# Kernel tuning notes

Measured on AMD Instinct MI355X. Metric: run time of the kernel, lower is better.

Reference implementation:

```python
import jax, jax.numpy as jnp
import numpy as np

V, E, H, D = 50257, 512, 512, 2  # vocab, embed_dim, hidden_dim, depth (nlayers)
B, S, T = 32, 60, 48             # batch, encoder len, target len


def setup_inputs() -> dict:
    key = jax.random.key(0)
    ks = jax.random.split(key, 9)
    return {
        "enc_h": jax.random.normal(ks[0], (B, S, 2 * H), jnp.float32),
        "prev_s": jax.random.normal(ks[1], (B, H), jnp.float32),
        "target": jax.random.randint(ks[2], (T, B), 0, V),
        "embed_W": jax.random.normal(ks[3], (V, E), jnp.float32) * 0.02,
        "attn_W": jax.random.normal(ks[4], (2 * H, H), jnp.float32) * (1.0 / np.sqrt(2 * H)),
        "attn_b": jnp.zeros((H,), jnp.float32),
        "inp_W": jax.random.normal(ks[5], (E, 2 * H), jnp.float32) * (1.0 / np.sqrt(E)),
        "inp_b": jnp.zeros((2 * H,), jnp.float32),
        "cell_W": jax.random.normal(ks[6], (D, H, 2 * H), jnp.float32) * (1.0 / np.sqrt(H)),
        "cell_b": jnp.zeros((D, 2 * H), jnp.float32),
        "out_W": jax.random.normal(ks[7], (H, V), jnp.float32) * (1.0 / np.sqrt(H)),
        "out_b": jnp.zeros((V,), jnp.float32),
    }


def reference(enc_h, prev_s, target, embed_W, attn_W, attn_b,
              inp_W, inp_b, cell_W, cell_b, out_W, out_b):
    # target: T x B -> embeddings T x B x E
    emb = embed_W[target]
    # enc_h is fixed across timesteps: precompute attention keys (B x S x H)
    energy = jnp.tanh(enc_h @ attn_W + attn_b)
    depth = cell_W.shape[0]

    def step(s, x_t):
        # attention: scores B x S, ctx B x 2H
        scores = jnp.einsum("bsh,bh->bs", energy, s)
        alpha = jax.nn.softmax(scores, axis=-1)
        ctx = jnp.einsum("bs,bsd->bd", alpha, enc_h)
        ctx_e = ctx[:, :E]  # module uses ctx[:, 0:embed_dim] (j never updated)
        for l in range(depth):  # small fixed depth loop
            Ws = (s * ctx_e) @ cell_W[l] + cell_b[l]
            if l == 0:
                Ws = Ws + x_t @ inp_W + inp_b
            hh, tt = jnp.split(Ws, 2, axis=1)
            hh = jnp.tanh(hh)
            tt = jax.nn.sigmoid(tt)
            s = hh * tt + s * (1.0 - tt)  # highway gate (dropout p=0)
        return s, s

    _, dec_h = jax.lax.scan(step, prev_s, emb)  # T x B x H
    return dec_h @ out_W + out_b  # T x B x V
```

## Files before the change

### kernel.cpp

```cpp
#include <hip/hip_runtime.h>
#include <hip/hip_bf16.h>
#include <math.h>

#define B_ 32
#define S_ 60
#define T_ 48
#define H_ 512
#define E_ 512
#define V_ 50257
#define NPAD 50432
#define EPI_LD 260

typedef __attribute__((ext_vector_type(8))) short bf16x8v;
typedef __attribute__((ext_vector_type(4))) float f32x4v;
typedef __attribute__((ext_vector_type(4))) float f32x4a __attribute__((aligned(4)));
typedef __attribute__((ext_vector_type(4))) unsigned int u32x4;

__device__ inline unsigned short f2bf(float f) {
    union { float f; unsigned u; } v; v.f = f;
    unsigned r = v.u + 0x7fffu + ((v.u >> 16) & 1u);
    return (unsigned short)(r >> 16);
}
__device__ inline float bflo(unsigned u) { return __uint_as_float(u << 16); }

__device__ inline void gload_lds16(const void* g, void* l) {
    __builtin_amdgcn_global_load_lds(
        (const __attribute__((address_space(1))) unsigned int*)g,
        (__attribute__((address_space(3))) unsigned int*)l, 16, 0, 0);
}

__device__ __forceinline__ u32x4 ld_cohx4(const void* p) {
    u32x4 r;
    asm volatile("global_load_dwordx4 %0, %1, off sc0 sc1"
                 : "=v"(r) : "v"(p) : "memory");
    return r;
}
__device__ __forceinline__ float ld_coh_f32(const float* p) {
    float r;
    asm volatile("global_load_dword %0, %1, off sc0 sc1\n\ts_waitcnt vmcnt(0)"
                 : "=v"(r) : "v"(p) : "memory");
    return r;
}
__device__ __forceinline__ float ld_coh_f32_nw(const float* p) {
    float r;
    asm volatile("global_load_dword %0, %1, off sc0 sc1"
                 : "=v"(r) : "v"(p) : "memory");
    return r;
}
__device__ __forceinline__ void st_coh_f32(float* p, float v) {
    asm volatile("global_store_dword %0, %1, off sc0 sc1"
                 :: "v"(p), "v"(v) : "memory");
}
__device__ __forceinline__ void st_coh_u16(unsigned short* p, unsigned int v) {
    asm volatile("global_store_short %0, %1, off sc0 sc1"
                 :: "v"(p), "v"(v) : "memory");
}
__device__ __forceinline__ void st_coh_u32(int* p, int v) {
    asm volatile("global_store_dword %0, %1, off sc0 sc1"
                 :: "v"(p), "v"(v) : "memory");
}
__device__ __forceinline__ int ld_coh_u32(const int* p) {
    int r;
    asm volatile("global_load_dword %0, %1, off sc0 sc1\n\ts_waitcnt vmcnt(0)"
                 : "=v"(r) : "v"(p) : "memory");
    return r;
}

__device__ __forceinline__ void gbar(int* flags, int idx, int bi) {
    asm volatile("s_waitcnt vmcnt(0)" ::: "memory");
    __syncthreads();
    if (threadIdx.x == 0)
        st_coh_u32(&flags[idx * 32 + bi], 1);
    if (threadIdx.x < 64) {
        const int* fp = &flags[idx * 32 + (threadIdx.x & 31)];
        for (;;) {
            int v = ld_coh_u32(fp);
            if (__all(v != 0)) break;
            __builtin_amdgcn_s_sleep(1);
        }
    }
    __syncthreads();
}

template<int ACT, bool GATHER>
__device__ void gemm_body(const float* __restrict__ A, const float* __restrict__ Bm,
                          const float* __restrict__ bias, float* __restrict__ C,
                          int N, int K, int lda, const int* __restrict__ gidx,
                          int cb, int rb, float (*As)[128], float (*Bs)[128])
{
    const int tid = threadIdx.x;
    const int am = tid >> 1;
    const int ak = (tid & 1) * 4;
    const int arow = rb + am;
    const float* Arow;
    if (GATHER) Arow = A + (size_t)gidx[arow] * lda;
    else        Arow = A + (size_t)arow * lda;

    const int bk = tid >> 5;
    const int bn = (tid & 31) * 4;

    const int tx = tid & 15, ty = tid >> 4;
    float acc[8][8];
    #pragma unroll
    for (int i = 0; i < 8; i++)
        #pragma unroll
        for (int j = 0; j < 8; j++) acc[i][j] = 0.f;

    for (int k0 = 0; k0 < K; k0 += 8) {
        float4 av = *(const float4*)(Arow + k0 + ak);
        float4 bv = *(const float4*)(Bm + (size_t)(k0 + bk) * N + cb + bn);
        __syncthreads();
        As[ak + 0][am] = av.x; As[ak + 1][am] = av.y;
        As[ak + 2][am] = av.z; As[ak + 3][am] = av.w;
        Bs[bk][bn + 0] = bv.x; Bs[bk][bn + 1] = bv.y;
        Bs[bk][bn + 2] = bv.z; Bs[bk][bn + 3] = bv.w;
        __syncthreads();

        #pragma unroll
        for (int k = 0; k < 8; k++) {
            float a[8], b[8];
            *(float4*)(a)     = *(const float4*)&As[k][ty * 4];
            *(float4*)(a + 4) = *(const float4*)&As[k][ty * 4 + 64];
            *(float4*)(b)     = *(const float4*)&Bs[k][tx * 4];
            *(float4*)(b + 4) = *(const float4*)&Bs[k][tx * 4 + 64];
            #pragma unroll
            for (int i = 0; i < 8; i++)
                #pragma unroll
                for (int j = 0; j < 8; j++)
                    acc[i][j] = fmaf(a[i], b[j], acc[i][j]);
        }
    }

    #pragma unroll
    for (int i = 0; i < 8; i++) {
        int row = rb + ((i < 4) ? (ty * 4 + i) : (64 + ty * 4 + (i - 4)));
        #pragma unroll
        for (int j = 0; j < 8; j++) {
            int col = cb + ((j < 4) ? (tx * 4 + j) : (64 + tx * 4 + (j - 4)));
            float v = acc[i][j] + bias[col];
            if (ACT == 1) v = tanhf(v);
            C[(size_t)row * N + col] = v;
        }
    }
}

__global__ __launch_bounds__(256)
void gemm_pro(const float* __restrict__ enc_h, const float* __restrict__ attn_W,
              const float* __restrict__ attn_b, float* __restrict__ energy,
              const float* __restrict__ embed_W, const float* __restrict__ inp_W,
              const float* __restrict__ inp_b, float* __restrict__ pre,
              const int* __restrict__ target, int* __restrict__ cnt)
{
    __shared__ float As[8][128];
    __shared__ float Bs[8][128];
    const int bx = blockIdx.x;
    if (bx < 60) {
        const int cb = (bx & 3) * 128, rb = (bx >> 2) * 128;
        gemm_body<1, false>(enc_h, attn_W, attn_b, energy,
                            512, 1024, 1024, nullptr, cb, rb, As, Bs);
    } else if (bx < 156) {
        const int b2 = bx - 60;
        const int cb = (b2 & 7) * 128, rb = (b2 >> 3) * 128;
        gemm_body<0, true>(embed_W, inp_W, inp_b, pre,
                           1024, 512, 512, target, cb, rb, As, Bs);
    } else {
        for (int i = threadIdx.x; i < 144 * 32; i += 256)
            st_coh_u32(&cnt[i], 0);
    }
}

union __align__(16) ScanSM {
    struct {
        float eL[S_][H_];
        float part[8 * 32 * 36];
        float sCol[512];
    } s;
    float til[2 * 32 * 33];
};

template<int LI>
__device__ __forceinline__ void highway(
    int t, int bi, int tid, int lane, int wv,
    const bf16x8v (&wf)[2][2],
    const unsigned short* __restrict__ xsrc,
    unsigned short* __restrict__ xG1,
    const float* __restrict__ ctxG,
    float* __restrict__ sG,
    unsigned short* __restrict__ dec_b,
    const float* __restrict__ pre,
    float cbh, float cbt,
    float* part, float* sCol)
{
    const int l15 = lane & 15, lc = lane >> 4;
    const int b = tid >> 4, hi = tid & 15;
    const int h = bi * 16 + hi;

    float cxv = 0.f, prh = 0.f, prt = 0.f;
    if (LI == 0) {
        cxv = ld_coh_f32_nw(ctxG + (size_t)b * 512 + h);
        const float* pr = pre + ((size_t)t * B_ + b) * 1024;
        prh = pr[h]; prt = pr[h + 512];
    }

    u32x4 xr[2][2][2];
    #pragma unroll
    for (int ktl = 0; ktl < 2; ++ktl)
        #pragma unroll
        for (int pl = 0; pl < 2; ++pl)
            #pragma unroll
            for (int mt = 0; mt < 2; ++mt) {
                int ch = (((wv * 2 + ktl) * 2 + pl) * 4 + lc) * 32 + mt * 16 + l15;
                xr[ktl][pl][mt] = ld_cohx4(xsrc + (size_t)ch * 8);
            }
    asm volatile("s_waitcnt vmcnt(0)" ::: "memory");
    __builtin_amdgcn_sched_barrier(0);

    f32x4v acc[2][2];
    #pragma unroll
    for (int mt = 0; mt < 2; ++mt)
        #pragma unroll
        for (int nt = 0; nt < 2; ++nt) acc[mt][nt] = (f32x4v)0.f;

    #pragma unroll
    for (int ktl = 0; ktl < 2; ++ktl)
        #pragma unroll
        for (int pl = 0; pl < 2; ++pl)
            #pragma unroll
            for (int mt = 0; mt < 2; ++mt) {
                bf16x8v xv = *(bf16x8v*)&xr[ktl][pl][mt];
                #pragma unroll
                for (int nt = 0; nt < 2; ++nt)
                    acc[mt][nt] = __builtin_amdgcn_mfma_f32_16x16x32_bf16(
                        wf[ktl][nt], xv, acc[mt][nt], 0, 0, 0);
            }

    #pragma unroll
    for (int mt = 0; mt < 2; ++mt)
        #pragma unroll
        for (int nt = 0; nt < 2; ++nt)
            *(f32x4v*)&part[(wv * 32 + mt * 16 + l15) * 36 + nt * 16 + lc * 4] = acc[mt][nt];
    __syncthreads();

    float rh = 0.f, rt = 0.f;
    #pragma unroll
    for (int w = 0; w < 8; ++w) {
        rh += part[(w * 32 + b) * 36 + hi];
        rt += part[(w * 32 + b) * 36 + 16 + hi];
    }
    float ph = rh + cbh, pt = rt + cbt;
    if (LI == 0) { ph += prh; pt += prt; }
    float hh = tanhf(ph);
    float tg = 1.f / (1.f + __expf(-pt));
    float sold = sCol[tid];
    float sn = hh * tg + sold * (1.f - tg);
    sCol[tid] = sn;
    if (LI == 0) {
        float x1 = sn * cxv;
        unsigned short xh = f2bf(x1);
        unsigned short xl = f2bf(x1 - bflo((unsigned)xh));
        int kt = h >> 5, lc2 = (h >> 3) & 3, jj = h & 7;
        int ch = (kt * 8 + lc2) * 32 + b;
        st_coh_u16(xG1 + (size_t)ch * 8 + jj, xh);
        st_coh_u16(xG1 + (size_t)(ch + 128) * 8 + jj, xl);
    } else {
        st_coh_f32(sG + ((size_t)bi * 32 + b) * 16 + hi, sn);
        dec_b[((size_t)bi * 1536 + (size_t)t * B_ + b) * 16 + hi] = f2bf(sn);
    }
}

__global__ __launch_bounds__(512, 2)
void scan_tr(const float* __restrict__ energy, const float* __restrict__ enc_h,
             const float* __restrict__ prev_s, const float* __restrict__ pre,
             const float* __restrict__ cell_W, const float* __restrict__ cell_b,
             unsigned short* __restrict__ dec_b,
             const float* __restrict__ outW, unsigned short* __restrict__ Wt,
             float* __restrict__ ctxG, float* __restrict__ sG,
             unsigned short* __restrict__ xG0, unsigned short* __restrict__ xG1,
             int* __restrict__ cnt)
{
    __shared__ ScanSM sm;
    const int tid = threadIdx.x;

    if (blockIdx.x >= B_) {
        const int hb = blockIdx.x - B_;
        const int g = tid >> 8;
        const int tt0 = tid & 255;
        const int r = tt0 >> 3, c4 = (tt0 & 7) * 4;
        float* til = sm.til;
        #pragma unroll 1
        for (int j = 0; j < 57; ++j) {
            const int tt = hb * 2 + g + j * 448;
            const bool act = tt < (NPAD / 32) * 16;
            int n0 = 0, k0 = 0;
            if (act) {
                n0 = (tt >> 4) * 32;
                k0 = (tt & 15) * 32;
                #pragma unroll
                for (int jj = 0; jj < 4; ++jj) {
                    int n = n0 + c4 + jj;
                    til[(g * 32 + r) * 33 + c4 + jj] =
                        (n < V_) ? __builtin_nontemporal_load(&outW[(size_t)(k0 + r) * V_ + n]) : 0.f;
                }
            }
            __syncthreads();
            if (act) {
                const int n = n0 + r;
                unsigned lo = (unsigned)f2bf(til[(g * 32 + c4 + 0) * 33 + r])
                            | ((unsigned)f2bf(til[(g * 32 + c4 + 1) * 33 + r]) << 16);
                unsigned hi2 = (unsigned)f2bf(til[(g * 32 + c4 + 2) * 33 + r])
                             | ((unsigned)f2bf(til[(g * 32 + c4 + 3) * 33 + r]) << 16);
                unsigned long long ov = (unsigned long long)lo | ((unsigned long long)hi2 << 32);
                __builtin_nontemporal_store(ov, (unsigned long long*)&Wt[(size_t)n * 512 + k0 + c4]);
            }
            __syncthreads();
        }
        return;
    }

    const int bi = blockIdx.x;
    const int lane = tid & 63, wv = tid >> 6;
    float (*eL)[H_] = sm.s.eL;
    float* part   = sm.s.part;
    float* sA     = part;
    float* scoreL = part + 512;
    float* alphaL = part + 576;
    float* sCol   = sm.s.sCol;
    int*   sF     = cnt + 100 * 32;

    for (int i = tid; i < S_ * H_ / 4; i += 512) {
        int s = i >> 7, h4 = (i & 127) * 4;
        *(float4*)&eL[s][h4] = *(const float4*)&energy[((size_t)bi * S_ + s) * 512 + h4];
    }

    bf16x8v wf0[2][2], wf1[2][2];
    {
        const int l15 = lane & 15, lc = lane >> 4;
        #pragma unroll
        for (int ktl = 0; ktl < 2; ++ktl)
            #pragma unroll
            for (int nt = 0; nt < 2; ++nt) {
                const int kb = (wv * 2 + ktl) * 32 + lc * 8;
                const int n  = nt * 512 + bi * 16 + l15;
                #pragma unroll
                for (int jj = 0; jj < 8; ++jj) {
                    wf0[ktl][nt][jj] = (short)f2bf(cell_W[((size_t)(kb + jj)) * 1024 + n]);
                    wf1[ktl][nt][jj] = (short)f2bf(cell_W[((size_t)(512 + kb + jj)) * 1024 + n]);
                }
            }
    }
    const int hME = bi * 16 + (tid & 15);
    sCol[tid] = prev_s[(size_t)(tid >> 4) * 512 + hME];
    const float cb0h = cell_b[hME],        cb0t = cell_b[512 + hME];
    const float cb1h = cell_b[1024 + hME], cb1t = cell_b[1536 + hME];

    #pragma unroll 1
    for (int t = 0; t < T_; ++t) {
        float sAv;
        if (t == 0) {
            sAv = prev_s[(size_t)bi * 512 + tid];
            __syncthreads();
            sA[tid] = sAv;
            __syncthreads();
        } else {
            const int* fp = &sF[tid >> 4];
            for (;;) {
                int v = ld_coh_u32(fp);
                if (v >= t) break;
                __builtin_amdgcn_s_sleep(1);
            }
            sAv = ld_coh_f32_nw(sG + ((size_t)(tid >> 4) * 32 + bi) * 16 + (tid & 15));
            __syncthreads();
            asm volatile("s_waitcnt vmcnt(0)" ::: "memory");
            sA[tid] = sAv;
            __syncthreads();
        }

        #pragma unroll 1
        for (int sp = 0; sp < 4; ++sp) {
            const int s0 = wv + sp * 16;
            const int s1 = s0 + 8;
            const bool has1 = (sp < 3) | (wv < 4);
            const float* e0 = &eL[s0][lane];
            const float* e1 = &eL[has1 ? s1 : s0][lane];
            float a0 = 0.f, a1 = 0.f;
            #pragma unroll
            for (int j = 0; j < 8; ++j) {
                float sv = sA[lane + j * 64];
                a0 = fmaf(e0[j * 64], sv, a0);
                a1 = fmaf(e1[j * 64], sv, a1);
            }
            #pragma unroll
            for (int off = 32; off; off >>= 1) {
                a0 += __shfl_xor(a0, off, 64);
                a1 += __shfl_xor(a1, off, 64);
            }
            if (lane == 0) {
                scoreL[s0] = a0;
                if (has1) scoreL[s1] = a1;
            }
        }
        __syncthreads();
        if (wv == 0) {
            float v = (lane < S_) ? scoreL[lane] : -3.4e38f;
            float m = v;
            #pragma unroll
            for (int off = 32; off; off >>= 1) m = fmaxf(m, __shfl_xor(m, off, 64));
            float e = (lane < S_) ? __expf(v - m) : 0.f;
            float su = e;
            #pragma unroll
            for (int off = 32; off; off >>= 1) su += __shfl_xor(su, off, 64);
            if (lane < S_) alphaL[lane] = e / su;
        }
        __syncthreads();
        {
            float a = 0.f;
            const float* ep = enc_h + (size_t)bi * S_ * 1024 + tid;
            #pragma unroll 20
            for (int s = 0; s < S_; ++s) a = fmaf(alphaL[s], ep[(size_t)s * 1024], a);
            st_coh_f32(ctxG + (size_t)bi * 512 + tid, a);
            float x0 = a * sA[tid];
            unsigned short xh = f2bf(x0);
            unsigned short xl = f2bf(x0 - bflo((unsigned)xh));
            int kt = tid >> 5, lc2 = (tid >> 3) & 3, jj = tid & 7;
            int ch = (kt * 8 + lc2) * 32 + bi;
            st_coh_u16(xG0 + (size_t)ch * 8 + jj, xh);
            st_coh_u16(xG0 + (size_t)(ch + 128) * 8 + jj, xl);
        }
        gbar(cnt, 2 * t + 0, bi);
        highway<0>(t, bi, tid, lane, wv, wf0, xG0, xG1, ctxG, sG, dec_b, pre,
                   cb0h, cb0t, part, sCol);
        gbar(cnt, 2 * t + 1, bi);
        highway<1>(t, bi, tid, lane, wv, wf1, xG1, xG1, ctxG, sG, dec_b, pre,
                   cb1h, cb1t, part, sCol);
        asm volatile("s_waitcnt vmcnt(0)" ::: "memory");
        __syncthreads();
        if (tid == 0)
            st_coh_u32(&sF[bi], t + 1);
    }
}

__global__ __launch_bounds__(512)
void gemm_out(const unsigned short* __restrict__ dec, const unsigned short* __restrict__ Wt,
              const float* __restrict__ bias, float* __restrict__ out)
{
    __shared__ char smem[49152];
    short* As_wt  = (short*)smem;
    short* Bs_dec = (short*)(smem + 32768);
    float* epi    = (float*)smem;

    const int tid = threadIdx.x;
    const int lane = tid & 63, w = tid >> 6;
    const int wm = w >> 2, wn = w & 3;

    const int nwg = (NPAD / 256) * 12;
    const int qx = nwg >> 3, rx = nwg & 7;
    const int xcd = blockIdx.x & 7, idx = blockIdx.x >> 3;
    const int wgid = (xcd < rx ? xcd * (qx + 1) : rx * (qx + 1) + (xcd - rx) * qx) + idx;
    const int rb = (wgid % 12) * 128;
    const int cb = (wgid / 12) * 256;

#define STAGE_TILE(bi, kt) do {                                               \
        short* Ab_ = As_wt + (bi) * 8192;                                     \
        short* Bb_ = Bs_dec + (bi) * 4096;                                    \
        _Pragma("unroll")                                                     \
        for (int j_ = 0; j_ < 2; ++j_) {                                      \
            int rg_ = w * 2 + j_;                                             \
            int row_ = rg_ * 16 + (lane >> 2);                                \
            int kc_ = (lane & 3) ^ (row_ & 3);                                \
            gload_lds16(Wt + ((size_t)(cb + row_) * 512 + (kt) * 32 + kc_ * 8), \
                        Ab_ + rg_ * 512);                                     \
        }                                                                     \
        {                                                                     \
            int row_ = w * 16 + (lane >> 2);                                  \
            int kc_ = (lane & 3) ^ (row_ & 3);                                \
            gload_lds16(dec + (((size_t)((kt) * 2 + (kc_ >> 1)) * 1536 + (rb + row_)) * 16 \
                               + (kc_ & 1) * 8),                              \
                        Bb_ + w * 512);                                       \
        }                                                                     \
    } while (0)

    f32x4v acc[4][4];
    #pragma unroll
    for (int i = 0; i < 4; ++i)
        #pragma unroll
        for (int j = 0; j < 4; ++j) acc[i][j] = (f32x4v)0.f;

    STAGE_TILE(0, 0);

    #pragma unroll 1
    for (int it = 0; it < 16; ++it) {
        const int cur = it & 1;
        __builtin_amdgcn_s_barrier();
        asm volatile("" ::: "memory");
        if (it < 15) {
            STAGE_TILE(cur ^ 1, it + 1);
            asm volatile("s_waitcnt vmcnt(3)" ::: "memory");
        } else {
            asm volatile("s_waitcnt vmcnt(0)" ::: "memory");
        }
        __builtin_amdgcn_s_barrier();
        asm volatile("" ::: "memory");

        const short* Ab = As_wt + cur * 8192;
        const short* Bb = Bs_dec + cur * 4096;
        bf16x8v af[4], bf[4];
        const int lc = lane >> 4;
        #pragma unroll
        for (int ni = 0; ni < 4; ++ni) {
            int r = wn * 64 + ni * 16 + (lane & 15);
            af[ni] = *(const bf16x8v*)&Ab[r * 32 + ((lc ^ (r & 3)) * 8)];
        }
        #pragma unroll
        for (int mi = 0; mi < 4; ++mi) {
            int r = wm * 64 + mi * 16 + (lane & 15);
            bf[mi] = *(const bf16x8v*)&Bb[r * 32 + ((lc ^ (r & 3)) * 8)];
        }
        #pragma unroll
        for (int mi = 0; mi < 4; ++mi)
            #pragma unroll
            for (int ni = 0; ni < 4; ++ni)
                acc[mi][ni] = __builtin_amdgcn_mfma_f32_16x16x32_bf16(
                    af[ni], bf[mi], acc[mi][ni], 0, 0, 0);
    }
#undef STAGE_TILE

    const int c4 = (tid & 63) * 4;
    const bool fullcols = (cb + 256 <= V_);
    f32x4v bq = (f32x4v)0.f;
    if (fullcols) {
        float4 t4 = *(const float4*)(bias + cb + c4);
        bq[0] = t4.x; bq[1] = t4.y; bq[2] = t4.z; bq[3] = t4.w;
    }

    #pragma unroll
    for (int mi = 0; mi < 4; ++mi) {
        __syncthreads();
        #pragma unroll
        for (int ni = 0; ni < 4; ++ni) {
            const int er = wm * 16 + (lane & 15);
            const int ec = wn * 64 + ni * 16 + (lane >> 4) * 4;
            *(f32x4v*)&epi[er * EPI_LD + ec] = acc[mi][ni];
        }
        __syncthreads();
        #pragma unroll
        for (int j = 0; j < 4; ++j) {
            const int rr = w + j * 8;
            const int orow = rb + (rr >> 4) * 64 + mi * 16 + (rr & 15);
            f32x4v v = *(const f32x4v*)&epi[rr * EPI_LD + c4];
            if (fullcols) {
                v += bq;
                *(f32x4a*)(out + (size_t)orow * V_ + cb + c4) = v;
            } else {
                #pragma unroll
                for (int vv = 0; vv < 4; ++vv) {
                    const int col = cb + c4 + vv;
                    if (col < V_)
                        out[(size_t)orow * V_ + col] = v[vv] + bias[col];
                }
            }
        }
    }
}

extern "C" void kernel_launch(void* const* d_in, const int* in_sizes, int n_in,
                              void* d_out, int out_size, void* d_ws, size_t ws_size,
                              hipStream_t stream)
{
    const float* enc_h   = (const float*)d_in[0];
    const float* prev_s  = (const float*)d_in[1];
    const int*   target  = (const int*)  d_in[2];
    const float* embed_W = (const float*)d_in[3];
    const float* attn_W  = (const float*)d_in[4];
    const float* attn_b  = (const float*)d_in[5];
    const float* inp_W   = (const float*)d_in[6];
    const float* inp_b   = (const float*)d_in[7];
    const float* cell_W  = (const float*)d_in[8];
    const float* cell_b  = (const float*)d_in[9];
    const float* out_W   = (const float*)d_in[10];
    const float* out_b   = (const float*)d_in[11];
    float* out = (float*)d_out;

    float* ws = (float*)d_ws;
    float* energy = ws;
    float* pre    = energy + (size_t)B_ * S_ * H_;
    float* ctxG   = pre + (size_t)T_ * B_ * 2 * H_;
    float* sG     = ctxG + (size_t)B_ * H_;
    int*   cnt    = (int*)(sG + (size_t)B_ * H_);
    unsigned short* dec_b = (unsigned short*)(cnt + 144 * 32);
    unsigned short* xG0   = dec_b + (size_t)T_ * B_ * H_;
    unsigned short* xG1   = xG0 + (size_t)2 * B_ * H_;
    unsigned short* Wt    = xG1 + (size_t)2 * B_ * H_;

    gemm_pro<<<157, 256, 0, stream>>>(enc_h, attn_W, attn_b, energy,
                                      embed_W, inp_W, inp_b, pre, target, cnt);

    scan_tr<<<256, 512, 0, stream>>>(energy, enc_h, prev_s, pre, cell_W, cell_b,
                                     dec_b, out_W, Wt, ctxG, sG, xG0, xG1, cnt);

    gemm_out<<<(NPAD / 256) * 12, 512, 0, stream>>>(dec_b, Wt, out_b, out);
}
```

Baseline: 902.5 us.

## Fuse output projection GEMM into scan kernel, overlapping with recurrent steps

The separate output GEMM kernel is removed. The 224 helper blocks of the scan kernel, after transposing out_W to bf16, synchronize among themselves and then compute output tiles. Each tile waits on the scan's per-timestep flags, so 128-row tiles of the projection run while later timesteps are still being processed. Loads switch from global_load_lds to coherent register loads staged through LDS, and dec_b/Wt stores become coherent. This hides the projection behind the latency-bound scan. The cost is only 224 workgroups for the GEMM, plus spin-wait overhead and possible contention with the scan blocks.

```diff
diff --git a/kernel.cpp b/kernel.cpp
--- a/kernel.cpp
+++ b/kernel.cpp
@@ -10,6 +10,7 @@
 #define V_ 50257
 #define NPAD 50432
 #define EPI_LD 260
+#define NTILE ((NPAD / 256) * 12)
 
 typedef __attribute__((ext_vector_type(8))) short bf16x8v;
 typedef __attribute__((ext_vector_type(4))) float f32x4v;
@@ -22,12 +23,6 @@
     return (unsigned short)(r >> 16);
 }
 __device__ inline float bflo(unsigned u) { return __uint_as_float(u << 16); }
-
-__device__ inline void gload_lds16(const void* g, void* l) {
-    __builtin_amdgcn_global_load_lds(
-        (const __attribute__((address_space(1))) unsigned int*)g,
-        (__attribute__((address_space(3))) unsigned int*)l, 16, 0, 0);
-}
 
 __device__ __forceinline__ u32x4 ld_cohx4(const void* p) {
     u32x4 r;
@@ -57,6 +52,10 @@
 }
 __device__ __forceinline__ void st_coh_u32(int* p, int v) {
     asm volatile("global_store_dword %0, %1, off sc0 sc1"
+                 :: "v"(p), "v"(v) : "memory");
+}
+__device__ __forceinline__ void st_coh_u64(unsigned long long* p, unsigned long long v) {
+    asm volatile("global_store_dwordx2 %0, %1, off sc0 sc1"
                  :: "v"(p), "v"(v) : "memory");
 }
 __device__ __forceinline__ int ld_coh_u32(const int* p) {
@@ -176,6 +175,7 @@
         float sCol[512];
     } s;
     float til[2 * 32 * 33];
+    char g[49152];
 };
 
 template<int LI>
@@ -264,7 +264,8 @@
         st_coh_u16(xG1 + (size_t)(ch + 128) * 8 + jj, xl);
     } else {
         st_coh_f32(sG + ((size_t)bi * 32 + b) * 16 + hi, sn);
-        dec_b[((size_t)bi * 1536 + (size_t)t * B_ + b) * 16 + hi] = f2bf(sn);
+        st_coh_u16(dec_b + ((size_t)bi * 1536 + (size_t)t * B_ + b) * 16 + hi,
+                   f2bf(sn));
     }
 }
 
@@ -276,7 +277,8 @@
              const float* __restrict__ outW, unsigned short* __restrict__ Wt,
              float* __restrict__ ctxG, float* __restrict__ sG,
              unsigned short* __restrict__ xG0, unsigned short* __restrict__ xG1,
-             int* __restrict__ cnt)
+             int* __restrict__ cnt,
+             const float* __restrict__ out_b, float* __restrict__ out)
 {
     __shared__ ScanSM sm;
     const int tid = threadIdx.x;
@@ -310,9 +312,169 @@
                 unsigned hi2 = (unsigned)f2bf(til[(g * 32 + c4 + 2) * 33 + r])
                              | ((unsigned)f2bf(til[(g * 32 + c4 + 3) * 33 + r]) << 16);
                 unsigned long long ov = (unsigned long long)lo | ((unsigned long long)hi2 << 32);
-                __builtin_nontemporal_store(ov, (unsigned long long*)&Wt[(size_t)n * 512 + k0 + c4]);
-            }
-            __syncthreads();
+                st_coh_u64((unsigned long long*)&Wt[(size_t)n * 512 + k0 + c4], ov);
+            }
+            __syncthreads();
+        }
+
+        {
+            int* hF = cnt + 101 * 32;
+            asm volatile("s_waitcnt vmcnt(0)" ::: "memory");
+            __syncthreads();
+            if (tid == 0) st_coh_u32(&hF[hb], 1);
+            if (tid < 64) {
+                for (;;) {
+                    int ok = 1;
+                    #pragma unroll
+                    for (int q = 0; q < 4; ++q) {
+                        int idx = (tid & 63) + q * 64;
+                        int v = (idx < 224) ? ld_coh_u32(&hF[idx]) : 1;
+                        ok &= (v != 0);
+                    }
+                    if (__all(ok)) break;
+                    __builtin_amdgcn_s_sleep(16);
+                }
+            }
+            __syncthreads();
+        }
+
+        {
+            short* As_wt  = (short*)sm.g;
+            short* Bs_dec = (short*)(sm.g + 32768);
+            float* epi    = (float*)sm.g;
+            const int lane = tid & 63, w = tid >> 6;
+            const int wm = w >> 2, wn = w & 3;
+            int* sF = cnt + 100 * 32;
+
+#define GISSUE(kt, rA0, rA1, rB) do {                                          \
+            int rowA0_ = (w * 2) * 16 + (lane >> 2);                           \
+            int rowA1_ = (w * 2 + 1) * 16 + (lane >> 2);                       \
+            int kcA0_ = (lane & 3) ^ (rowA0_ & 3);                             \
+            int kcA1_ = (lane & 3) ^ (rowA1_ & 3);                             \
+            rA0 = ld_cohx4(Wt + ((size_t)(cb + rowA0_) * 512 + (kt) * 32 + kcA0_ * 8)); \
+            rA1 = ld_cohx4(Wt + ((size_t)(cb + rowA1_) * 512 + (kt) * 32 + kcA1_ * 8)); \
+            int rowB_ = w * 16 + (lane >> 2);                                  \
+            int kcB_ = (lane & 3) ^ (rowB_ & 3);                               \
+            rB = ld_cohx4(dec_b + (((size_t)((kt) * 2 + (kcB_ >> 1)) * 1536 + (rb + rowB_)) * 16 \
+                                   + (kcB_ & 1) * 8));                         \
+        } while (0)
+
+#define GWRITE(bix, rA0, rA1, rB) do {                                         \
+            short* Ab_ = As_wt + (bix) * 8192;                                 \
+            short* Bb_ = Bs_dec + (bix) * 4096;                                \
+            *(u32x4*)&Ab_[(w * 2) * 512 + lane * 8] = rA0;                     \
+            *(u32x4*)&Ab_[(w * 2 + 1) * 512 + lane * 8] = rA1;                 \
+            *(u32x4*)&Bb_[w * 512 + lane * 8] = rB;                            \
+        } while (0)
+
+#define GCOMPUTE(bix) do {                                                     \
+            const short* Ab_ = As_wt + (bix) * 8192;                           \
+            const short* Bb_ = Bs_dec + (bix) * 4096;                          \
+            bf16x8v af[4], bf[4];                                              \
+            const int lc_ = lane >> 4;                                         \
+            _Pragma("unroll")                                                  \
+            for (int ni = 0; ni < 4; ++ni) {                                   \
+                int r_ = wn * 64 + ni * 16 + (lane & 15);                      \
+                af[ni] = *(const bf16x8v*)&Ab_[r_ * 32 + ((lc_ ^ (r_ & 3)) * 8)]; \
+            }                                                                  \
+            _Pragma("unroll")                                                  \
+            for (int mi = 0; mi < 4; ++mi) {                                   \
+                int r_ = wm * 64 + mi * 16 + (lane & 15);                      \
+                bf[mi] = *(const bf16x8v*)&Bb_[r_ * 32 + ((lc_ ^ (r_ & 3)) * 8)]; \
+            }                                                                  \
+            _Pragma("unroll")                                                  \
+            for (int mi = 0; mi < 4; ++mi)                                     \
+                _Pragma("unroll")                                              \
+                for (int ni = 0; ni < 4; ++ni)                                 \
+                    acc[mi][ni] = __builtin_amdgcn_mfma_f32_16x16x32_bf16(     \
+                        af[ni], bf[mi], acc[mi][ni], 0, 0, 0);                 \
+        } while (0)
+
+            #pragma unroll 1
+            for (int i = hb; i < NTILE; i += 224) {
+                const int rbi = i / 197;
+                const int rb  = rbi * 128;
+                const int cb  = (i % 197) * 256;
+                const int need = rbi * 4 + 4;
+
+                if (tid < 64) {
+                    const int* fp = &sF[tid & 31];
+                    for (;;) {
+                        int v = ld_coh_u32(fp);
+                        if (__all(v >= need)) break;
+                        __builtin_amdgcn_s_sleep(32);
+                    }
+                }
+                __syncthreads();
+
+                f32x4v acc[4][4];
+                #pragma unroll
+                for (int mi = 0; mi < 4; ++mi)
+                    #pragma unroll
+                    for (int ni = 0; ni < 4; ++ni) acc[mi][ni] = (f32x4v)0.f;
+
+                u32x4 eA0, eA1, eB, oA0, oA1, oB;
+                GISSUE(0, eA0, eA1, eB);
+                GISSUE(1, oA0, oA1, oB);
+
+                #pragma unroll 1
+                for (int p = 0; p < 8; ++p) {
+                    asm volatile("s_waitcnt vmcnt(3)" ::: "memory");
+                    __syncthreads();
+                    GWRITE(0, eA0, eA1, eB);
+                    asm volatile("s_waitcnt lgkmcnt(0)" ::: "memory");
+                    if (p < 7) GISSUE(2 * p + 2, eA0, eA1, eB);
+                    __syncthreads();
+                    GCOMPUTE(0);
+                    if (p < 7) asm volatile("s_waitcnt vmcnt(3)" ::: "memory");
+                    else       asm volatile("s_waitcnt vmcnt(0)" ::: "memory");
+                    __syncthreads();
+                    GWRITE(1, oA0, oA1, oB);
+                    asm volatile("s_waitcnt lgkmcnt(0)" ::: "memory");
+                    if (p < 7) GISSUE(2 * p + 3, oA0, oA1, oB);
+                    __syncthreads();
+                    GCOMPUTE(1);
+                }
+
+                const int c4e = (tid & 63) * 4;
+                const bool fullcols = (cb + 256 <= V_);
+                f32x4v bq = (f32x4v)0.f;
+                if (fullcols) {
+                    float4 t4 = *(const float4*)(out_b + cb + c4e);
+                    bq[0] = t4.x; bq[1] = t4.y; bq[2] = t4.z; bq[3] = t4.w;
+                }
+                #pragma unroll
+                for (int mi = 0; mi < 4; ++mi) {
+                    __syncthreads();
+                    #pragma unroll
+                    for (int ni = 0; ni < 4; ++ni) {
+                        const int er = wm * 16 + (lane & 15);
+                        const int ec = wn * 64 + ni * 16 + (lane >> 4) * 4;
+                        *(f32x4v*)&epi[er * EPI_LD + ec] = acc[mi][ni];
+                    }
+                    __syncthreads();
+                    #pragma unroll
+                    for (int j = 0; j < 4; ++j) {
+                        const int rr = w + j * 8;
+                        const int orow = rb + (rr >> 4) * 64 + mi * 16 + (rr & 15);
+                        f32x4v v = *(const f32x4v*)&epi[rr * EPI_LD + c4e];
+                        if (fullcols) {
+                            v += bq;
+                            *(f32x4a*)(out + (size_t)orow * V_ + cb + c4e) = v;
+                        } else {
+                            #pragma unroll
+                            for (int vv = 0; vv < 4; ++vv) {
+                                const int col = cb + c4e + vv;
+                                if (col < V_)
+                                    out[(size_t)orow * V_ + col] = v[vv] + out_b[col];
+                            }
+                        }
+                    }
+                }
+            }
+#undef GISSUE
+#undef GWRITE
+#undef GCOMPUTE
         }
         return;
     }
@@ -436,129 +598,6 @@
         __syncthreads();
         if (tid == 0)
             st_coh_u32(&sF[bi], t + 1);
-    }
-}
-
-__global__ __launch_bounds__(512)
-void gemm_out(const unsigned short* __restrict__ dec, const unsigned short* __restrict__ Wt,
-              const float* __restrict__ bias, float* __restrict__ out)
-{
-    __shared__ char smem[49152];
-    short* As_wt  = (short*)smem;
-    short* Bs_dec = (short*)(smem + 32768);
-    float* epi    = (float*)smem;
-
-    const int tid = threadIdx.x;
-    const int lane = tid & 63, w = tid >> 6;
-    const int wm = w >> 2, wn = w & 3;
-
-    const int nwg = (NPAD / 256) * 12;
-    const int qx = nwg >> 3, rx = nwg & 7;
-    const int xcd = blockIdx.x & 7, idx = blockIdx.x >> 3;
-    const int wgid = (xcd < rx ? xcd * (qx + 1) : rx * (qx + 1) + (xcd - rx) * qx) + idx;
-    const int rb = (wgid % 12) * 128;
-    const int cb = (wgid / 12) * 256;
-
-#define STAGE_TILE(bi, kt) do {                                               \
-        short* Ab_ = As_wt + (bi) * 8192;                                     \
-        short* Bb_ = Bs_dec + (bi) * 4096;                                    \
-        _Pragma("unroll")                                                     \
-        for (int j_ = 0; j_ < 2; ++j_) {                                      \
-            int rg_ = w * 2 + j_;                                             \
-            int row_ = rg_ * 16 + (lane >> 2);                                \
-            int kc_ = (lane & 3) ^ (row_ & 3);                                \
-            gload_lds16(Wt + ((size_t)(cb + row_) * 512 + (kt) * 32 + kc_ * 8), \
-                        Ab_ + rg_ * 512);                                     \
-        }                                                                     \
-        {                                                                     \
-            int row_ = w * 16 + (lane >> 2);                                  \
-            int kc_ = (lane & 3) ^ (row_ & 3);                                \
-            gload_lds16(dec + (((size_t)((kt) * 2 + (kc_ >> 1)) * 1536 + (rb + row_)) * 16 \
-                               + (kc_ & 1) * 8),                              \
-                        Bb_ + w * 512);                                       \
-        }                                                                     \
-    } while (0)
-
-    f32x4v acc[4][4];
-    #pragma unroll
-    for (int i = 0; i < 4; ++i)
-        #pragma unroll
-        for (int j = 0; j < 4; ++j) acc[i][j] = (f32x4v)0.f;
-
-    STAGE_TILE(0, 0);
-
-    #pragma unroll 1
-    for (int it = 0; it < 16; ++it) {
-        const int cur = it & 1;
-        __builtin_amdgcn_s_barrier();
-        asm volatile("" ::: "memory");
-        if (it < 15) {
-            STAGE_TILE(cur ^ 1, it + 1);
-            asm volatile("s_waitcnt vmcnt(3)" ::: "memory");
-        } else {
-            asm volatile("s_waitcnt vmcnt(0)" ::: "memory");
-        }
-        __builtin_amdgcn_s_barrier();
-        asm volatile("" ::: "memory");
-
-        const short* Ab = As_wt + cur * 8192;
-        const short* Bb = Bs_dec + cur * 4096;
-        bf16x8v af[4], bf[4];
-        const int lc = lane >> 4;
-        #pragma unroll
-        for (int ni = 0; ni < 4; ++ni) {
-            int r = wn * 64 + ni * 16 + (lane & 15);
-            af[ni] = *(const bf16x8v*)&Ab[r * 32 + ((lc ^ (r & 3)) * 8)];
-        }
-        #pragma unroll
-        for (int mi = 0; mi < 4; ++mi) {
-            int r = wm * 64 + mi * 16 + (lane & 15);
-            bf[mi] = *(const bf16x8v*)&Bb[r * 32 + ((lc ^ (r & 3)) * 8)];
-        }
-        #pragma unroll
-        for (int mi = 0; mi < 4; ++mi)
-            #pragma unroll
-            for (int ni = 0; ni < 4; ++ni)
-                acc[mi][ni] = __builtin_amdgcn_mfma_f32_16x16x32_bf16(
-                    af[ni], bf[mi], acc[mi][ni], 0, 0, 0);
-    }
-#undef STAGE_TILE
-
-    const int c4 = (tid & 63) * 4;
-    const bool fullcols = (cb + 256 <= V_);
-    f32x4v bq = (f32x4v)0.f;
-    if (fullcols) {
-        float4 t4 = *(const float4*)(bias + cb + c4);
-        bq[0] = t4.x; bq[1] = t4.y; bq[2] = t4.z; bq[3] = t4.w;
-    }
-
-    #pragma unroll
-    for (int mi = 0; mi < 4; ++mi) {
-        __syncthreads();
-        #pragma unroll
-        for (int ni = 0; ni < 4; ++ni) {
-            const int er = wm * 16 + (lane & 15);
-            const int ec = wn * 64 + ni * 16 + (lane >> 4) * 4;
-            *(f32x4v*)&epi[er * EPI_LD + ec] = acc[mi][ni];
-        }
-        __syncthreads();
-        #pragma unroll
-        for (int j = 0; j < 4; ++j) {
-            const int rr = w + j * 8;
-            const int orow = rb + (rr >> 4) * 64 + mi * 16 + (rr & 15);
-            f32x4v v = *(const f32x4v*)&epi[rr * EPI_LD + c4];
-            if (fullcols) {
-                v += bq;
-                *(f32x4a*)(out + (size_t)orow * V_ + cb + c4) = v;
-            } else {
-                #pragma unroll
-                for (int vv = 0; vv < 4; ++vv) {
-                    const int col = cb + c4 + vv;
-                    if (col < V_)
-                        out[(size_t)orow * V_ + col] = v[vv] + bias[col];
-                }
-            }
-        }
     }
 }
 
@@ -595,7 +634,6 @@
                                       embed_W, inp_W, inp_b, pre, target, cnt);
 
     scan_tr<<<256, 512, 0, stream>>>(energy, enc_h, prev_s, pre, cell_W, cell_b,
-                                     dec_b, out_W, Wt, ctxG, sG, xG0, xG1, cnt);
-
-    gemm_out<<<(NPAD / 256) * 12, 512, 0, stream>>>(dec_b, Wt, out_b, out);
-}
+                                     dec_b, out_W, Wt, ctxG, sG, xG0, xG1, cnt,
+                                     out_b, out);
+}
```

New measurement: 845.8 us. 1.07x faster.
